# Optimization experiments

Measured on AMD Instinct MI355X. Metric: run time of the kernel, lower is better.

Reference implementation:

```python
import jax, jax.numpy as jnp
import numpy as np
import math

H = 128
NUM_RBF = 32
CUTOFF_UPPER = 4.5
CUTOFF_LOWER = 0.0
N_NODES = 16384
N_EDGES = 65536
EPS = 1e-5


def _layernorm(x, gamma, beta):
    m = x.mean(-1, keepdims=True)
    v = ((x - m) ** 2).mean(-1, keepdims=True)
    return (x - m) / jnp.sqrt(v + EPS) * gamma + beta


def _cosine_cutoff(d):
    # cutoff_lower == 0 branch of CosineCutoff
    return 0.5 * (jnp.cos(d * (math.pi / CUTOFF_UPPER)) + 1.0) * (d < CUTOFF_UPPER).astype(d.dtype)


def _expnorm_rbf(d):
    alpha = 5.0 / (CUTOFF_UPPER - CUTOFF_LOWER)
    start = math.exp(-CUTOFF_UPPER + CUTOFF_LOWER)
    means = jnp.linspace(start, 1.0, NUM_RBF, dtype=d.dtype)
    betas = jnp.full((NUM_RBF,), (2.0 / NUM_RBF * (1.0 - start)) ** -2, dtype=d.dtype)
    de = d[:, None]
    return _cosine_cutoff(de) * jnp.exp(-betas * (jnp.exp(alpha * (-de + CUTOFF_LOWER)) - means) ** 2)


def _skew(v):  # [E,3] -> [E,3,3]
    z = jnp.zeros(v.shape[0], v.dtype)
    return jnp.stack([z, -v[:, 2], v[:, 1], v[:, 2], z, -v[:, 0], -v[:, 1], v[:, 0], z], axis=1).reshape(-1, 3, 3)


def _sym(v):  # traceless symmetric part of outer product, [E,3] -> [E,3,3]
    M = v[:, :, None] * v[:, None, :]
    tr3 = (v * v).sum(-1)[:, None, None] / 3.0
    return M - tr3 * jnp.eye(3, dtype=v.dtype)


def _tensor_norm(T):  # [...,3,3] -> [...]
    return (T ** 2).sum((-2, -1))


def setup_inputs() -> dict:
    key = jax.random.key(0)
    ks = jax.random.split(key, 32)
    s = 0.05
    inp = {
        'z': jax.random.randint(ks[0], (N_NODES,), 0, 128, dtype=jnp.int32),
        'pos': jax.random.normal(ks[1], (N_NODES, 3), jnp.float32) * 3.0,
        'batch': jnp.zeros((N_NODES,), jnp.int32),
        'edge_index': jax.random.randint(ks[2], (2, N_EDGES), 0, N_NODES, dtype=jnp.int64),
        'emb_w': jax.random.normal(ks[3], (128, H), jnp.float32) * s,
        'emb2_w': jax.random.normal(ks[4], (H, 2 * H), jnp.float32) * s,
        'emb2_b': jnp.zeros((H,), jnp.float32),
        'dp1_w': jax.random.normal(ks[5], (H, NUM_RBF), jnp.float32) * s,
        'dp1_b': jnp.zeros((H,), jnp.float32),
        'dp2_w': jax.random.normal(ks[6], (H, NUM_RBF), jnp.float32) * s,
        'dp2_b': jnp.zeros((H,), jnp.float32),
        'dp3_w': jax.random.normal(ks[7], (H, NUM_RBF), jnp.float32) * s,
        'dp3_b': jnp.zeros((H,), jnp.float32),
        'lt0_w': jax.random.normal(ks[8], (H, H), jnp.float32) * s,
        'lt1_w': jax.random.normal(ks[9], (H, H), jnp.float32) * s,
        'lt2_w': jax.random.normal(ks[10], (H, H), jnp.float32) * s,
        'ls0_w': jax.random.normal(ks[11], (2 * H, H), jnp.float32) * s,
        'ls0_b': jnp.zeros((2 * H,), jnp.float32),
        'ls1_w': jax.random.normal(ks[12], (3 * H, 2 * H), jnp.float32) * s,
        'ls1_b': jnp.zeros((3 * H,), jnp.float32),
        'in_gamma': jnp.ones((H,), jnp.float32),
        'in_beta': jnp.zeros((H,), jnp.float32),
        'lin_w': jax.random.normal(ks[13], (H, 3 * H), jnp.float32) * s,
        'lin_b': jnp.zeros((H,), jnp.float32),
        'on_gamma': jnp.ones((3 * H,), jnp.float32),
        'on_beta': jnp.zeros((3 * H,), jnp.float32),
        'ol1_w': jax.random.normal(ks[14], (H // 2, H), jnp.float32) * s,
        'ol1_b': jnp.zeros((H // 2,), jnp.float32),
        'ol2_w': jax.random.normal(ks[15], (1, H // 2), jnp.float32) * s,
        'ol2_b': jnp.zeros((1,), jnp.float32),
    }
    return inp


def reference(z, pos, batch, edge_index, emb_w, emb2_w, emb2_b, dp1_w, dp1_b, dp2_w, dp2_b,
              dp3_w, dp3_b, lt0_w, lt1_w, lt2_w, ls0_w, ls0_b, ls1_w, ls1_b,
              in_gamma, in_beta, lin_w, lin_b, on_gamma, on_beta, ol1_w, ol1_b, ol2_w, ol2_b):
    src, dst = edge_index[0], edge_index[1]
    edge_vec = pos[src] - pos[dst]                            # [E,3]
    edge_weight = jnp.sqrt((edge_vec ** 2).sum(-1))           # [E]
    edge_attr = _expnorm_rbf(edge_weight)                     # [E,R]
    self_mask = src == dst
    edge_vec_norm = edge_vec / jnp.where(self_mask, 1.0, edge_weight)[:, None]

    # atomic-number message: Zij = emb2(concat(emb[z_src], emb[z_dst]))
    Zemb = emb_w[z]                                           # [N,H]
    Zcat = jnp.concatenate([Zemb[src], Zemb[dst]], axis=-1)   # [E,2H]
    Zij = Zcat @ emb2_w.T + emb2_b                            # [E,H]

    C = (_cosine_cutoff(edge_weight)[:, None] * Zij)[:, :, None, None]  # [E,H,1,1]
    eye = jnp.eye(3, dtype=pos.dtype)[None, None]
    d1 = (edge_attr @ dp1_w.T + dp1_b)[:, :, None, None]      # [E,H,1,1]
    d2 = (edge_attr @ dp2_w.T + dp2_b)[:, :, None, None]
    d3 = (edge_attr @ dp3_w.T + dp3_b)[:, :, None, None]
    Iij = d1 * C * eye                                        # [E,H,3,3]
    Aij = d2 * C * _skew(edge_vec_norm)[:, None, :, :]
    Sij = d3 * C * _sym(edge_vec_norm)[:, None, :, :]

    N = pos.shape[0]
    I0 = jax.ops.segment_sum(Iij, src, num_segments=N)        # [N,H,3,3]
    A0 = jax.ops.segment_sum(Aij, src, num_segments=N)
    S0 = jax.ops.segment_sum(Sij, src, num_segments=N)

    tnorm = _layernorm(_tensor_norm(I0 + A0 + S0), in_gamma, in_beta)  # [N,H]
    nrm = jax.nn.silu(tnorm @ ls0_w.T + ls0_b)
    nrm = jax.nn.silu(nrm @ ls1_w.T + ls1_b).reshape(-1, H, 3)          # [N,H,3]

    I = jnp.einsum('nhij,kh->nkij', I0, lt0_w) * nrm[:, :, 0, None, None]
    A = jnp.einsum('nhij,kh->nkij', A0, lt1_w) * nrm[:, :, 1, None, None]
    S = jnp.einsum('nhij,kh->nkij', S0, lt2_w) * nrm[:, :, 2, None, None]

    x = jnp.concatenate([_tensor_norm(I), _tensor_norm(A), _tensor_norm(S)], axis=-1)  # [N,3H]
    x = _layernorm(x, on_gamma, on_beta)
    x = jax.nn.silu(x @ lin_w.T + lin_b)                       # [N,H]
    x = jax.nn.silu(x @ ol1_w.T + ol1_b)                       # [N,H//2]
    y = x @ ol2_w.T + ol2_b                                    # [N,1] per-atom scalar
    return y
```

## Files before the change

### kernel.cpp

```cpp
#include <hip/hip_runtime.h>
#include <math.h>

#define NN 16384
#define NE 65536
#define HH 128

constexpr double D_START = 0.011108996538242306;
constexpr double D_STEP  = (1.0 - D_START) / 31.0;
constexpr float  F_ALPHA = (float)(5.0/4.5);
constexpr double D_BB    = (2.0/32.0)*(1.0 - D_START);
constexpr float  F_BETA  = (float)(1.0/(D_BB*D_BB));
constexpr float  F_PIC   = (float)(M_PI/4.5);

#define POOL_BYTES (16u*1024u*1024u)
__device__ __align__(256) static char g_pool[POOL_BYTES];

typedef __attribute__((ext_vector_type(8))) short bf16x8;
typedef __attribute__((ext_vector_type(4))) float f32x4;

__device__ __forceinline__ float siluf(float x){
  return x * (1.0f/(1.0f + expf(-x)));
}
__device__ __forceinline__ short f2bf(float x){
  unsigned u = __float_as_uint(x);
  unsigned r = (u + 0x7fffu + ((u>>16)&1u)) >> 16;
  return (short)r;
}
__device__ __forceinline__ float bf2f(short h){
  return __uint_as_float(((unsigned)(unsigned short)h)<<16);
}
__device__ __forceinline__ void split_bf(float x, short& h, short& l){
  h = f2bf(x);
  l = f2bf(x - bf2f(h));
}

__global__ __launch_bounds__(256) void k_prep(
    const int* __restrict__ ei, const float* __restrict__ pos,
    const int* __restrict__ z,
    const float* __restrict__ emb_w, const float* __restrict__ emb2_w,
    const float* __restrict__ emb2_b,
    const float* __restrict__ ls0, const float* __restrict__ ls1,
    const float* __restrict__ lin, const float* __restrict__ lt0,
    const float* __restrict__ lt1, const float* __restrict__ lt2,
    const float* __restrict__ dp1, const float* __restrict__ dp2,
    const float* __restrict__ dp3, const float* __restrict__ ol1,
    float* __restrict__ PZ, float* __restrict__ QZ,
    int* __restrict__ bcnt, int* __restrict__ bucket,
    int* __restrict__ ezs, int* __restrict__ ezd, float* __restrict__ ev,
    short* __restrict__ atth, short* __restrict__ attl,
    short* __restrict__ ls0h, short* __restrict__ ls0l,
    short* __restrict__ ls1h, short* __restrict__ ls1l,
    short* __restrict__ linh, short* __restrict__ linl,
    short* __restrict__ lt0h, short* __restrict__ lt0l,
    short* __restrict__ lt1h, short* __restrict__ lt1l,
    short* __restrict__ lt2h, short* __restrict__ lt2l,
    short* __restrict__ dwh, short* __restrict__ dwl,
    short* __restrict__ ol1h, short* __restrict__ ol1l){
  int b = blockIdx.x;
  if (b < 64){
    __shared__ float erow[2][128];
    int sub = threadIdx.x >> 7, h = threadIdx.x & 127;
    int a = b*2 + sub;
    erow[sub][h] = emb_w[a*128 + h];
    __syncthreads();
    float p = 0.f, q = 0.f;
    #pragma unroll 8
    for (int k=0;k<128;++k){
      float e = erow[sub][k];
      p += e * emb2_w[h*256 + k];
      q += e * emb2_w[h*256 + 128 + k];
    }
    PZ[a*128 + h] = p + emb2_b[h];
    QZ[a*128 + h] = q;
    return;
  }
  if (b < 1040){
    int tid = (b-64)*256 + threadIdx.x;
    const float* s; short *dh, *dl; int i;
    if      (tid < 32768)  { s=ls0; dh=ls0h; dl=ls0l; i=tid; }
    else if (tid < 131072) { s=ls1; dh=ls1h; dl=ls1l; i=tid-32768; }
    else if (tid < 180224) { s=lin; dh=linh; dl=linl; i=tid-131072; }
    else if (tid < 196608) { s=lt0; dh=lt0h; dl=lt0l; i=tid-180224; }
    else if (tid < 212992) { s=lt1; dh=lt1h; dl=lt1l; i=tid-196608; }
    else if (tid < 229376) { s=lt2; dh=lt2h; dl=lt2l; i=tid-212992; }
    else if (tid < 241664) {
      int j = tid - 229376;
      int g = j >> 12, idx = j & 4095;
      s = (g==0)?dp1:((g==1)?dp2:dp3);
      short h,l; split_bf(s[idx], h, l);
      dwh[j] = h; dwl[j] = l;
      return;
    }
    else { s=ol1; dh=ol1h; dl=ol1l; i=tid-241664; }
    short h,l; split_bf(s[i], h, l);
    dh[i] = h; dl[i] = l;
    return;
  }
  {
    int e = (b-1040)*256 + threadIdx.x;
    int s = ei[e];
    int t = ei[NE + e];
    float dx = pos[3*s+0] - pos[3*t+0];
    float dy = pos[3*s+1] - pos[3*t+1];
    float dz = pos[3*s+2] - pos[3*t+2];
    float d = sqrtf(dx*dx + dy*dy + dz*dz);
    if (d < 4.5f){
      int g16 = s >> 4;
      int p = atomicAdd(&bcnt[g16], 1);
      if (p < 512) bucket[g16*512 + p] = (e<<4) | (s & 15);
      ezs[e] = z[s];
      ezd[e] = z[t];
      float denom = (s==t) ? 1.0f : d;
      ev[4*e+0] = dx/denom;
      ev[4*e+1] = dy/denom;
      ev[4*e+2] = dz/denom;
      float cut = 0.5f*(cosf(d*F_PIC) + 1.0f);
      ev[4*e+3] = cut;
      float q = expf(-F_ALPHA*d);
      #pragma unroll
      for (int r=0;r<32;++r){
        float m = (float)(D_START + r*D_STEP);
        float u = q - m;
        float a = cut * expf(-F_BETA*u*u);
        short hh, ll; split_bf(a, hh, ll);
        atth[32*e + r] = hh;
        attl[32*e + r] = ll;
      }
    }
  }
}

__global__ __launch_bounds__(256, 2) void k_mega(
    const int* __restrict__ bcnt, const int* __restrict__ bucket,
    const int* __restrict__ ezs, const int* __restrict__ ezd,
    const float* __restrict__ ev,
    const short* __restrict__ atth, const short* __restrict__ attl,
    const short* __restrict__ dwh, const short* __restrict__ dwl,
    const float* __restrict__ db1, const float* __restrict__ db2,
    const float* __restrict__ db3,
    const float* __restrict__ PZ, const float* __restrict__ QZ,
    const float* __restrict__ in_g, const float* __restrict__ in_b,
    const short* __restrict__ w0h, const short* __restrict__ w0l,
    const short* __restrict__ w1h, const short* __restrict__ w1l,
    const short* __restrict__ w2h, const short* __restrict__ w2l,
    const short* __restrict__ ls0h, const short* __restrict__ ls0l,
    const float* __restrict__ ls0b,
    const short* __restrict__ ls1h, const short* __restrict__ ls1l,
    const float* __restrict__ ls1b,
    const short* __restrict__ linh, const short* __restrict__ linl,
    const float* __restrict__ linb,
    const short* __restrict__ ol1h, const short* __restrict__ ol1l,
    const float* __restrict__ ol1b,
    const float* __restrict__ ol2w, const float* __restrict__ ol2b,
    const float* __restrict__ on_g, const float* __restrict__ on_b,
    float* __restrict__ y){
  __shared__ __align__(16) char sm[76288];
  float* Dt    = (float*)sm;
  int*   elocal= (int*)(sm + 24832);
  int*   tmpb  = (int*)(sm + 26880);
  int*   lcnt  = (int*)(sm + 28928);
  int*   loff  = lcnt + 16;
  int*   lcur  = loff + 17;
  short* PlnL  = (short*)sm;
  short* T1h   = (short*)sm;
  short* T1l   = (short*)(sm + 9216);
  float* xls   = (float*)sm;
  short* X3h   = (short*)sm;
  short* X3l   = (short*)(sm + 5120);
  float* partL = (float*)(sm + 10240);
  short* tnhL  = (short*)(sm + 51200);
  short* tnlL  = (short*)(sm + 51200 + 5120);
  float* NRMt  = (float*)(sm + 51200);
  short* xhL   = (short*)(sm + 51200);
  short* xlL   = (short*)(sm + 51200 + 12544);

  int t = threadIdx.x;
  int b = blockIdx.x;
  int w = t >> 6, lane = t & 63;
  int col16 = lane & 15, quad = lane >> 4;
  int bn = b*16;
  int node = t >> 4, q = t & 15;

  int ecnt = bcnt[b]; if (ecnt > 512) ecnt = 512;
  if (t < 16){ lcnt[t] = 0; lcur[t] = 0; }
  __syncthreads();
  for (int j = t; j < ecnt; j += 256){
    int val = bucket[b*512 + j];
    tmpb[j] = val;
    atomicAdd(&lcnt[val & 15], 1);
  }
  __syncthreads();
  if (t == 0){
    int a = 0;
    #pragma unroll
    for (int i=0;i<16;++i){ loff[i] = a; a += lcnt[i]; }
    loff[16] = a;
  }
  __syncthreads();
  for (int j = t; j < ecnt; j += 256){
    int val = tmpb[j];
    int nd = val & 15;
    int p = loff[nd] + atomicAdd(&lcur[nd], 1);
    elocal[p] = val >> 4;
  }
  __syncthreads();
  int etot = loff[16];
  int e0n = loff[node], e1n = loff[node+1];

  float pv[10][8];
  #pragma unroll
  for (int p=0;p<10;++p)
    #pragma unroll
    for (int i=0;i<8;++i) pv[p][i]=0.f;

  const float* dbp[3] = {db1, db2, db3};
  for (int c0 = 0; c0 < etot; c0 += 16){
    int jA = c0 + col16; if (jA >= etot) jA = etot - 1;
    int eA = elocal[jA];
    bf16x8 ah = *(const bf16x8*)(atth + (size_t)eA*32 + quad*8);
    bf16x8 al = *(const bf16x8*)(attl + (size_t)eA*32 + quad*8);
    f32x4 dacc[6];
    #pragma unroll
    for (int nt=0;nt<6;++nt) dacc[nt] = (f32x4){0.f,0.f,0.f,0.f};
    #pragma unroll
    for (int nt=0;nt<6;++nt){
      int col = w*96 + nt*16 + col16;
      int g = col >> 7, cg = col & 127;
      bf16x8 wh = *(const bf16x8*)(dwh + g*4096 + cg*32 + quad*8);
      bf16x8 wl = *(const bf16x8*)(dwl + g*4096 + cg*32 + quad*8);
      dacc[nt] = __builtin_amdgcn_mfma_f32_16x16x32_bf16(ah, wh, dacc[nt], 0,0,0);
      dacc[nt] = __builtin_amdgcn_mfma_f32_16x16x32_bf16(ah, wl, dacc[nt], 0,0,0);
      dacc[nt] = __builtin_amdgcn_mfma_f32_16x16x32_bf16(al, wh, dacc[nt], 0,0,0);
    }
    #pragma unroll
    for (int nt=0;nt<6;++nt){
      int col = w*96 + nt*16 + col16;
      int g = col >> 7;
      float bb = dbp[g][col & 127];
      #pragma unroll
      for (int r=0;r<4;++r)
        Dt[(quad*4+r)*388 + col] = dacc[nt][r] + bb;
    }
    __syncthreads();
    int jlo = e0n > c0 ? e0n : c0;
    int jhi0 = c0 + 16; if (jhi0 > etot) jhi0 = etot;
    int jhi = e1n < jhi0 ? e1n : jhi0;
    for (int j = jlo; j < jhi; ++j){
      int le = j - c0;
      int e = elocal[j];
      float4 evv = *(const float4*)(ev + 4*e);
      int zs = ezs[e], zd = ezd[e];
      const float* pz = PZ + zs*128 + q*8;
      const float* qz = QZ + zd*128 + q*8;
      const float* dr = Dt + le*388 + q*8;
      float vx = evv.x, vy = evv.y, vz = evv.z, cut = evv.w;
      float t3v = (vx*vx + vy*vy + vz*vz)*(1.0f/3.0f);
      #pragma unroll
      for (int i=0;i<8;++i){
        float C = cut * (pz[i] + qz[i]);
        float d1 = dr[i], d2 = dr[128+i], d3 = dr[256+i];
        pv[0][i] += d1*C;
        float wa = d2*C;
        pv[1][i] += wa*vx; pv[2][i] += wa*vy; pv[3][i] += wa*vz;
        float ws = d3*C;
        pv[4][i] += ws*(vx*vx - t3v);
        pv[5][i] += ws*(vy*vy - t3v);
        pv[6][i] += ws*(vz*vz - t3v);
        pv[7][i] += ws*(vx*vy);
        pv[8][i] += ws*(vx*vz);
        pv[9][i] += ws*(vy*vz);
      }
    }
    __syncthreads();
  }

  {
    float tnv[8];
    float s8 = 0.f;
    #pragma unroll
    for (int i=0;i<8;++i){
      float x = 3.f*pv[0][i]*pv[0][i]
              + 2.f*(pv[1][i]*pv[1][i]+pv[2][i]*pv[2][i]+pv[3][i]*pv[3][i])
              + (pv[4][i]*pv[4][i]+pv[5][i]*pv[5][i]+pv[6][i]*pv[6][i])
              + 2.f*(pv[7][i]*pv[7][i]+pv[8][i]*pv[8][i]+pv[9][i]*pv[9][i]);
      tnv[i] = x; s8 += x;
    }
    #pragma unroll
    for (int o=8;o;o>>=1) s8 += __shfl_xor(s8, o, 64);
    float mean = s8*(1.0f/128.0f);
    float vq = 0.f;
    #pragma unroll
    for (int i=0;i<8;++i){ float d = tnv[i]-mean; vq += d*d; }
    #pragma unroll
    for (int o=8;o;o>>=1) vq += __shfl_xor(vq, o, 64);
    float rstd = 1.0f/sqrtf(vq*(1.0f/128.0f) + 1e-5f);
    #pragma unroll
    for (int i=0;i<8;++i){
      int h = q*8 + i;
      float val = (tnv[i]-mean)*rstd*in_g[h] + in_b[h];
      short hh, ll; split_bf(val, hh, ll);
      tnhL[node*160 + h] = hh;
      tnlL[node*160 + h] = ll;
    }
  }

  const short* wgh[3] = {w0h, w1h, w2h};
  const short* wgl[3] = {w0l, w1l, w2l};
  constexpr int gmap[10] = {0,1,1,1,2,2,2,2,2,2};
  f32x4 acc[10][2];
  #pragma unroll
  for (int pass=0; pass<2; ++pass){
    int pbase = pass*5;
    __syncthreads();
    #pragma unroll
    for (int pl=0; pl<5; ++pl){
      short* dst = PlnL + (pl*4 + (q>>2))*1280 + node*80 + (q&3)*16;
      #pragma unroll
      for (int i=0;i<8;++i){
        short hh, ll; split_bf(pv[pbase+pl][i], hh, ll);
        dst[i] = hh; dst[8+i] = ll;
      }
    }
    __syncthreads();
    #pragma unroll
    for (int pl=0; pl<5; ++pl)
      #pragma unroll
      for (int tt=0; tt<2; ++tt) acc[pbase+pl][tt] = (f32x4){0.f,0.f,0.f,0.f};
    #pragma unroll
    for (int hc4=0; hc4<4; ++hc4){
      bf16x8 bh[2], bl[2];
      int curg = -1;
      #pragma unroll
      for (int pl=0; pl<5; ++pl){
        int p = pbase + pl;
        const int g = gmap[p];
        if (g != curg){
          #pragma unroll
          for (int tt=0; tt<2; ++tt){
            int row = w*32 + tt*16 + col16;
            bh[tt] = *(const bf16x8*)(wgh[g] + row*128 + hc4*32 + quad*8);
            bl[tt] = *(const bf16x8*)(wgl[g] + row*128 + hc4*32 + quad*8);
          }
          curg = g;
        }
        const short* ab = PlnL + (pl*4 + hc4)*1280 + col16*80 + quad*16;
        bf16x8 ah = *(const bf16x8*)(ab);
        bf16x8 al = *(const bf16x8*)(ab + 8);
        #pragma unroll
        for (int tt=0; tt<2; ++tt){
          acc[p][tt] = __builtin_amdgcn_mfma_f32_16x16x32_bf16(ah, bh[tt], acc[p][tt], 0,0,0);
          acc[p][tt] = __builtin_amdgcn_mfma_f32_16x16x32_bf16(ah, bl[tt], acc[p][tt], 0,0,0);
          acc[p][tt] = __builtin_amdgcn_mfma_f32_16x16x32_bf16(al, bh[tt], acc[p][tt], 0,0,0);
        }
      }
    }
  }
  __syncthreads();

  {
    f32x4 macc[4];
    #pragma unroll
    for (int nt=0;nt<4;++nt) macc[nt] = (f32x4){0.f,0.f,0.f,0.f};
    #pragma unroll
    for (int kc=0; kc<4; ++kc){
      bf16x8 tah = *(const bf16x8*)(tnhL + col16*160 + kc*32 + quad*8);
      bf16x8 tal = *(const bf16x8*)(tnlL + col16*160 + kc*32 + quad*8);
      #pragma unroll
      for (int nt=0;nt<4;++nt){
        int n = w*64 + nt*16 + col16;
        bf16x8 wh = *(const bf16x8*)(ls0h + n*128 + kc*32 + quad*8);
        bf16x8 wl = *(const bf16x8*)(ls0l + n*128 + kc*32 + quad*8);
        macc[nt] = __builtin_amdgcn_mfma_f32_16x16x32_bf16(tah, wh, macc[nt], 0,0,0);
        macc[nt] = __builtin_amdgcn_mfma_f32_16x16x32_bf16(tah, wl, macc[nt], 0,0,0);
        macc[nt] = __builtin_amdgcn_mfma_f32_16x16x32_bf16(tal, wh, macc[nt], 0,0,0);
      }
    }
    __syncthreads();
    #pragma unroll
    for (int nt=0;nt<4;++nt){
      int n = w*64 + nt*16 + col16;
      float bb = ls0b[n];
      #pragma unroll
      for (int r=0;r<4;++r){
        float v = siluf(macc[nt][r] + bb);
        short hh, ll; split_bf(v, hh, ll);
        T1h[(quad*4+r)*288 + n] = hh;
        T1l[(quad*4+r)*288 + n] = ll;
      }
    }
    __syncthreads();
    f32x4 nacc[6];
    #pragma unroll
    for (int nt=0;nt<6;++nt) nacc[nt] = (f32x4){0.f,0.f,0.f,0.f};
    #pragma unroll
    for (int kc=0; kc<8; ++kc){
      bf16x8 tah = *(const bf16x8*)(T1h + col16*288 + kc*32 + quad*8);
      bf16x8 tal = *(const bf16x8*)(T1l + col16*288 + kc*32 + quad*8);
      #pragma unroll
      for (int nt=0;nt<6;++nt){
        int n = w*96 + nt*16 + col16;
        bf16x8 wh = *(const bf16x8*)(ls1h + n*256 + kc*32 + quad*8);
        bf16x8 wl = *(const bf16x8*)(ls1l + n*256 + kc*32 + quad*8);
        nacc[nt] = __builtin_amdgcn_mfma_f32_16x16x32_bf16(tah, wh, nacc[nt], 0,0,0);
        nacc[nt] = __builtin_amdgcn_mfma_f32_16x16x32_bf16(tah, wl, nacc[nt], 0,0,0);
        nacc[nt] = __builtin_amdgcn_mfma_f32_16x16x32_bf16(tal, wh, nacc[nt], 0,0,0);
      }
    }
    __syncthreads();
    #pragma unroll
    for (int nt=0;nt<6;++nt){
      int n = w*96 + nt*16 + col16;
      float bb = ls1b[n];
      #pragma unroll
      for (int r=0;r<4;++r)
        NRMt[(quad*4+r)*388 + n] = siluf(nacc[nt][r] + bb);
    }
    __syncthreads();
  }

  #pragma unroll
  for (int tt=0; tt<2; ++tt){
    int k = w*32 + tt*16 + col16;
    #pragma unroll
    for (int r=0; r<4; ++r){
      int nloc = quad*4 + r;
      const float* nr = NRMt + nloc*388 + 3*k;
      float n0 = nr[0], n1 = nr[1], n2 = nr[2];
      float tI = acc[0][tt][r]*n0;
      float xI = 3.f*tI*tI;
      float a0 = acc[1][tt][r]*n1, a1 = acc[2][tt][r]*n1, a2 = acc[3][tt][r]*n1;
      float xA = 2.f*(a0*a0 + a1*a1 + a2*a2);
      float d0 = acc[4][tt][r]*n2, d1 = acc[5][tt][r]*n2, d2 = acc[6][tt][r]*n2;
      float o0 = acc[7][tt][r]*n2, o1 = acc[8][tt][r]*n2, o2 = acc[9][tt][r]*n2;
      float xS = d0*d0 + d1*d1 + d2*d2 + 2.f*(o0*o0 + o1*o1 + o2*o2);
      xls[nloc*388 + k]       = xI;
      xls[nloc*388 + 128 + k] = xA;
      xls[nloc*388 + 256 + k] = xS;
    }
  }
  __syncthreads();

  {
    float vv[24];
    float s = 0.f;
    #pragma unroll
    for (int i=0;i<24;++i){ vv[i] = xls[node*388 + q*24 + i]; s += vv[i]; }
    #pragma unroll
    for (int o=8;o;o>>=1) s += __shfl_xor(s, o, 64);
    float mean = s*(1.0f/384.0f);
    float qsum = 0.f;
    #pragma unroll
    for (int i=0;i<24;++i){ float d = vv[i]-mean; qsum += d*d; }
    #pragma unroll
    for (int o=8;o;o>>=1) qsum += __shfl_xor(qsum, o, 64);
    float rstd = 1.0f/sqrtf(qsum*(1.0f/384.0f) + 1e-5f);
    #pragma unroll
    for (int i=0;i<24;++i){
      int c = q*24 + i;
      float val = (vv[i]-mean)*rstd*on_g[c] + on_b[c];
      short hh, ll; split_bf(val, hh, ll);
      xhL[node*392 + c] = hh;
      xlL[node*392 + c] = ll;
    }
  }
  __syncthreads();

  {
    f32x4 lacc[2];
    #pragma unroll
    for (int nt=0;nt<2;++nt) lacc[nt] = (f32x4){0.f,0.f,0.f,0.f};
    #pragma unroll
    for (int kc=0; kc<12; ++kc){
      bf16x8 xah = *(const bf16x8*)(xhL + col16*392 + kc*32 + quad*8);
      bf16x8 xal = *(const bf16x8*)(xlL + col16*392 + kc*32 + quad*8);
      #pragma unroll
      for (int nt=0;nt<2;++nt){
        int n = w*32 + nt*16 + col16;
        bf16x8 wh = *(const bf16x8*)(linh + n*384 + kc*32 + quad*8);
        bf16x8 wl = *(const bf16x8*)(linl + n*384 + kc*32 + quad*8);
        lacc[nt] = __builtin_amdgcn_mfma_f32_16x16x32_bf16(xah, wh, lacc[nt], 0,0,0);
        lacc[nt] = __builtin_amdgcn_mfma_f32_16x16x32_bf16(xah, wl, lacc[nt], 0,0,0);
        lacc[nt] = __builtin_amdgcn_mfma_f32_16x16x32_bf16(xal, wh, lacc[nt], 0,0,0);
      }
    }
    __syncthreads();
    #pragma unroll
    for (int nt=0;nt<2;++nt){
      int n = w*32 + nt*16 + col16;
      float bb = linb[n];
      #pragma unroll
      for (int r=0;r<4;++r){
        float v = siluf(lacc[nt][r] + bb);
        short hh, ll; split_bf(v, hh, ll);
        X3h[(quad*4+r)*160 + n] = hh;
        X3l[(quad*4+r)*160 + n] = ll;
      }
    }
    __syncthreads();
  }

  {
    f32x4 hacc = (f32x4){0.f,0.f,0.f,0.f};
    int n = w*16 + col16;
    #pragma unroll
    for (int kc=0; kc<4; ++kc){
      bf16x8 xah = *(const bf16x8*)(X3h + col16*160 + kc*32 + quad*8);
      bf16x8 xal = *(const bf16x8*)(X3l + col16*160 + kc*32 + quad*8);
      bf16x8 wh = *(const bf16x8*)(ol1h + n*128 + kc*32 + quad*8);
      bf16x8 wl = *(const bf16x8*)(ol1l + n*128 + kc*32 + quad*8);
      hacc = __builtin_amdgcn_mfma_f32_16x16x32_bf16(xah, wh, hacc, 0,0,0);
      hacc = __builtin_amdgcn_mfma_f32_16x16x32_bf16(xah, wl, hacc, 0,0,0);
      hacc = __builtin_amdgcn_mfma_f32_16x16x32_bf16(xal, wh, hacc, 0,0,0);
    }
    float b1 = ol1b[n], w2 = ol2w[n];
    #pragma unroll
    for (int r=0;r<4;++r){
      float v = siluf(hacc[r] + b1) * w2;
      #pragma unroll
      for (int o=8;o;o>>=1) v += __shfl_xor(v, o, 64);
      if (col16 == 0) partL[w*16 + quad*4 + r] = v;
    }
    __syncthreads();
    if (t < 16)
      y[bn + t] = partL[t] + partL[16+t] + partL[32+t] + partL[48+t] + ol2b[0];
  }
}

extern "C" void kernel_launch(void* const* d_in, const int* in_sizes, int n_in,
                              void* d_out, int out_size, void* d_ws, size_t ws_size,
                              hipStream_t stream) {
  const int*   z      = (const int*)d_in[0];
  const float* pos    = (const float*)d_in[1];
  const int*   ei     = (const int*)d_in[3];
  const float* emb_w  = (const float*)d_in[4];
  const float* emb2_w = (const float*)d_in[5];
  const float* emb2_b = (const float*)d_in[6];
  const float* dp1_w  = (const float*)d_in[7];
  const float* dp1_b  = (const float*)d_in[8];
  const float* dp2_w  = (const float*)d_in[9];
  const float* dp2_b  = (const float*)d_in[10];
  const float* dp3_w  = (const float*)d_in[11];
  const float* dp3_b  = (const float*)d_in[12];
  const float* lt0_w  = (const float*)d_in[13];
  const float* lt1_w  = (const float*)d_in[14];
  const float* lt2_w  = (const float*)d_in[15];
  const float* ls0_w  = (const float*)d_in[16];
  const float* ls0_b  = (const float*)d_in[17];
  const float* ls1_w  = (const float*)d_in[18];
  const float* ls1_b  = (const float*)d_in[19];
  const float* in_g   = (const float*)d_in[20];
  const float* in_b   = (const float*)d_in[21];
  const float* lin_w  = (const float*)d_in[22];
  const float* lin_b  = (const float*)d_in[23];
  const float* on_g   = (const float*)d_in[24];
  const float* on_b   = (const float*)d_in[25];
  const float* ol1_w  = (const float*)d_in[26];
  const float* ol1_b  = (const float*)d_in[27];
  const float* ol2_w  = (const float*)d_in[28];
  const float* ol2_b  = (const float*)d_in[29];
  float* out = (float*)d_out;

  const size_t NEED = 14u*1024u*1024u;
  char* wsb = (char*)d_ws;
  if (ws_size < NEED){
    void* p = nullptr;
    hipGetSymbolAddress(&p, HIP_SYMBOL(g_pool));
    wsb = (char*)p;
  }
  size_t off = 0;
  auto alloc = [&](size_t bytes)->void*{
    void* p = wsb + off;
    off = (off + bytes + 255) & ~(size_t)255;
    return p;
  };
  float* PZ      = (float*)alloc(128*128*4);
  float* QZ      = (float*)alloc(128*128*4);
  int*   bcnt    = (int*)  alloc(1024*4);
  int*   bucket  = (int*)  alloc((size_t)1024*512*4);
  int*   ezs     = (int*)  alloc(NE*4);
  int*   ezd     = (int*)  alloc(NE*4);
  float* ev      = (float*)alloc((size_t)NE*4*4);
  short* atth    = (short*)alloc((size_t)NE*32*2);
  short* attl    = (short*)alloc((size_t)NE*32*2);
  short* dwh     = (short*)alloc(3*128*32*2);
  short* dwl     = (short*)alloc(3*128*32*2);
  short* ls0h    = (short*)alloc(256*128*2);
  short* ls0l    = (short*)alloc(256*128*2);
  short* ls1h    = (short*)alloc(384*256*2);
  short* ls1l    = (short*)alloc(384*256*2);
  short* linh    = (short*)alloc(128*384*2);
  short* linl    = (short*)alloc(128*384*2);
  short* lt0h    = (short*)alloc(128*128*2);
  short* lt0l    = (short*)alloc(128*128*2);
  short* lt1h    = (short*)alloc(128*128*2);
  short* lt1l    = (short*)alloc(128*128*2);
  short* lt2h    = (short*)alloc(128*128*2);
  short* lt2l    = (short*)alloc(128*128*2);
  short* ol1h    = (short*)alloc(64*128*2);
  short* ol1l    = (short*)alloc(64*128*2);

  hipMemsetAsync(bcnt, 0, 1024*4, stream);

  k_prep<<<1296, 256, 0, stream>>>(ei, pos, z, emb_w, emb2_w, emb2_b,
                                   ls0_w, ls1_w, lin_w, lt0_w, lt1_w, lt2_w,
                                   dp1_w, dp2_w, dp3_w, ol1_w,
                                   PZ, QZ, bcnt, bucket, ezs, ezd, ev, atth, attl,
                                   ls0h, ls0l, ls1h, ls1l, linh, linl,
                                   lt0h, lt0l, lt1h, lt1l, lt2h, lt2l,
                                   dwh, dwl, ol1h, ol1l);
  k_mega<<<NN/16, 256, 0, stream>>>(bcnt, bucket, ezs, ezd, ev, atth, attl,
                                    dwh, dwl, dp1_b, dp2_b, dp3_b,
                                    PZ, QZ, in_g, in_b,
                                    lt0h, lt0l, lt1h, lt1l, lt2h, lt2l,
                                    ls0h, ls0l, ls0_b, ls1h, ls1l, ls1_b,
                                    linh, linl, lin_b, ol1h, ol1l, ol1_b,
                                    ol2_w, ol2_b, on_g, on_b, out);
}
```

Baseline: 266.9 us.

## Reorder norm MLP before tensor GEMMs to shrink LDS and registers

Moves the ls0/ls1 MLP that produces the norm factors ahead of the per-component tensor linear GEMMs. Each GEMM pass's accumulators can then be reduced immediately into running xI/xA/xS sums instead of keeping all 10 accumulator planes live. Shared memory drops from about 76KB to 53KB by overlapping buffers, and launch bounds go from 2 to 3 blocks per CU to raise occupancy. The cost is five plane-staging passes instead of two, so more barriers, and register pressure may force spills.

```diff
diff --git a/kernel.cpp b/kernel.cpp
--- a/kernel.cpp
+++ b/kernel.cpp
@@ -130,7 +130,7 @@
   }
 }
 
-__global__ __launch_bounds__(256, 2) void k_mega(
+__global__ __launch_bounds__(256, 3) void k_mega(
     const int* __restrict__ bcnt, const int* __restrict__ bucket,
     const int* __restrict__ ezs, const int* __restrict__ ezd,
     const float* __restrict__ ev,
@@ -154,25 +154,25 @@
     const float* __restrict__ ol2w, const float* __restrict__ ol2b,
     const float* __restrict__ on_g, const float* __restrict__ on_b,
     float* __restrict__ y){
-  __shared__ __align__(16) char sm[76288];
+  __shared__ __align__(16) char sm[53248];
   float* Dt    = (float*)sm;
   int*   elocal= (int*)(sm + 24832);
-  int*   tmpb  = (int*)(sm + 26880);
-  int*   lcnt  = (int*)(sm + 28928);
+  int*   lcnt  = (int*)(sm + 26880);
   int*   loff  = lcnt + 16;
   int*   lcur  = loff + 17;
-  short* PlnL  = (short*)sm;
   short* T1h   = (short*)sm;
   short* T1l   = (short*)(sm + 9216);
+  short* PlnL  = (short*)sm;
   float* xls   = (float*)sm;
   short* X3h   = (short*)sm;
   short* X3l   = (short*)(sm + 5120);
   float* partL = (float*)(sm + 10240);
-  short* tnhL  = (short*)(sm + 51200);
-  short* tnlL  = (short*)(sm + 51200 + 5120);
-  float* NRMt  = (float*)(sm + 51200);
-  short* xhL   = (short*)(sm + 51200);
-  short* xlL   = (short*)(sm + 51200 + 12544);
+  int*   tmpb  = (int*)(sm + 28160);
+  short* tnhL  = (short*)(sm + 28160);
+  short* tnlL  = (short*)(sm + 28160 + 5120);
+  float* NRMt  = (float*)(sm + 28160);
+  short* xhL   = (short*)(sm + 28160);
+  short* xlL   = (short*)(sm + 28160 + 12544);
 
   int t = threadIdx.x;
   int b = blockIdx.x;
@@ -303,17 +303,80 @@
       tnlL[node*160 + h] = ll;
     }
   }
+  __syncthreads();
+
+  {
+    f32x4 macc[4];
+    #pragma unroll
+    for (int nt=0;nt<4;++nt) macc[nt] = (f32x4){0.f,0.f,0.f,0.f};
+    #pragma unroll
+    for (int kc=0; kc<4; ++kc){
+      bf16x8 tah = *(const bf16x8*)(tnhL + col16*160 + kc*32 + quad*8);
+      bf16x8 tal = *(const bf16x8*)(tnlL + col16*160 + kc*32 + quad*8);
+      #pragma unroll
+      for (int nt=0;nt<4;++nt){
+        int n = w*64 + nt*16 + col16;
+        bf16x8 wh = *(const bf16x8*)(ls0h + n*128 + kc*32 + quad*8);
+        bf16x8 wl = *(const bf16x8*)(ls0l + n*128 + kc*32 + quad*8);
+        macc[nt] = __builtin_amdgcn_mfma_f32_16x16x32_bf16(tah, wh, macc[nt], 0,0,0);
+        macc[nt] = __builtin_amdgcn_mfma_f32_16x16x32_bf16(tah, wl, macc[nt], 0,0,0);
+        macc[nt] = __builtin_amdgcn_mfma_f32_16x16x32_bf16(tal, wh, macc[nt], 0,0,0);
+      }
+    }
+    #pragma unroll
+    for (int nt=0;nt<4;++nt){
+      int n = w*64 + nt*16 + col16;
+      float bb = ls0b[n];
+      #pragma unroll
+      for (int r=0;r<4;++r){
+        float v = siluf(macc[nt][r] + bb);
+        short hh, ll; split_bf(v, hh, ll);
+        T1h[(quad*4+r)*288 + n] = hh;
+        T1l[(quad*4+r)*288 + n] = ll;
+      }
+    }
+    __syncthreads();
+    f32x4 nacc[6];
+    #pragma unroll
+    for (int nt=0;nt<6;++nt) nacc[nt] = (f32x4){0.f,0.f,0.f,0.f};
+    #pragma unroll
+    for (int kc=0; kc<8; ++kc){
+      bf16x8 tah = *(const bf16x8*)(T1h + col16*288 + kc*32 + quad*8);
+      bf16x8 tal = *(const bf16x8*)(T1l + col16*288 + kc*32 + quad*8);
+      #pragma unroll
+      for (int nt=0;nt<6;++nt){
+        int n = w*96 + nt*16 + col16;
+        bf16x8 wh = *(const bf16x8*)(ls1h + n*256 + kc*32 + quad*8);
+        bf16x8 wl = *(const bf16x8*)(ls1l + n*256 + kc*32 + quad*8);
+        nacc[nt] = __builtin_amdgcn_mfma_f32_16x16x32_bf16(tah, wh, nacc[nt], 0,0,0);
+        nacc[nt] = __builtin_amdgcn_mfma_f32_16x16x32_bf16(tah, wl, nacc[nt], 0,0,0);
+        nacc[nt] = __builtin_amdgcn_mfma_f32_16x16x32_bf16(tal, wh, nacc[nt], 0,0,0);
+      }
+    }
+    __syncthreads();
+    #pragma unroll
+    for (int nt=0;nt<6;++nt){
+      int n = w*96 + nt*16 + col16;
+      float bb = ls1b[n];
+      #pragma unroll
+      for (int r=0;r<4;++r)
+        NRMt[(quad*4+r)*388 + n] = siluf(nacc[nt][r] + bb);
+    }
+  }
 
   const short* wgh[3] = {w0h, w1h, w2h};
   const short* wgl[3] = {w0l, w1l, w2l};
-  constexpr int gmap[10] = {0,1,1,1,2,2,2,2,2,2};
-  f32x4 acc[10][2];
+  float xI[2][4], xA[2][4], xS[2][4];
   #pragma unroll
-  for (int pass=0; pass<2; ++pass){
-    int pbase = pass*5;
-    __syncthreads();
-    #pragma unroll
-    for (int pl=0; pl<5; ++pl){
+  for (int tt=0;tt<2;++tt)
+    #pragma unroll
+    for (int r=0;r<4;++r){ xI[tt][r]=0.f; xA[tt][r]=0.f; xS[tt][r]=0.f; }
+  #pragma unroll
+  for (int pass=0; pass<5; ++pass){
+    const int pbase = pass*2;
+    __syncthreads();
+    #pragma unroll
+    for (int pl=0; pl<2; ++pl){
       short* dst = PlnL + (pl*4 + (q>>2))*1280 + node*80 + (q&3)*16;
       #pragma unroll
       for (int i=0;i<8;++i){
@@ -322,18 +385,19 @@
       }
     }
     __syncthreads();
-    #pragma unroll
-    for (int pl=0; pl<5; ++pl)
-      #pragma unroll
-      for (int tt=0; tt<2; ++tt) acc[pbase+pl][tt] = (f32x4){0.f,0.f,0.f,0.f};
+    f32x4 acc[2][2];
+    #pragma unroll
+    for (int pl=0;pl<2;++pl)
+      #pragma unroll
+      for (int tt=0;tt<2;++tt) acc[pl][tt] = (f32x4){0.f,0.f,0.f,0.f};
     #pragma unroll
     for (int hc4=0; hc4<4; ++hc4){
       bf16x8 bh[2], bl[2];
       int curg = -1;
       #pragma unroll
-      for (int pl=0; pl<5; ++pl){
-        int p = pbase + pl;
-        const int g = gmap[p];
+      for (int pl=0; pl<2; ++pl){
+        const int p = pbase + pl;
+        const int g = (p==0)?0:((p<4)?1:2);
         if (g != curg){
           #pragma unroll
           for (int tt=0; tt<2; ++tt){
@@ -348,75 +412,33 @@
         bf16x8 al = *(const bf16x8*)(ab + 8);
         #pragma unroll
         for (int tt=0; tt<2; ++tt){
-          acc[p][tt] = __builtin_amdgcn_mfma_f32_16x16x32_bf16(ah, bh[tt], acc[p][tt], 0,0,0);
-          acc[p][tt] = __builtin_amdgcn_mfma_f32_16x16x32_bf16(ah, bl[tt], acc[p][tt], 0,0,0);
-          acc[p][tt] = __builtin_amdgcn_mfma_f32_16x16x32_bf16(al, bh[tt], acc[p][tt], 0,0,0);
+          acc[pl][tt] = __builtin_amdgcn_mfma_f32_16x16x32_bf16(ah, bh[tt], acc[pl][tt], 0,0,0);
+          acc[pl][tt] = __builtin_amdgcn_mfma_f32_16x16x32_bf16(ah, bl[tt], acc[pl][tt], 0,0,0);
+          acc[pl][tt] = __builtin_amdgcn_mfma_f32_16x16x32_bf16(al, bh[tt], acc[pl][tt], 0,0,0);
         }
       }
     }
-  }
-  __syncthreads();
-
-  {
-    f32x4 macc[4];
-    #pragma unroll
-    for (int nt=0;nt<4;++nt) macc[nt] = (f32x4){0.f,0.f,0.f,0.f};
-    #pragma unroll
-    for (int kc=0; kc<4; ++kc){
-      bf16x8 tah = *(const bf16x8*)(tnhL + col16*160 + kc*32 + quad*8);
-      bf16x8 tal = *(const bf16x8*)(tnlL + col16*160 + kc*32 + quad*8);
-      #pragma unroll
-      for (int nt=0;nt<4;++nt){
-        int n = w*64 + nt*16 + col16;
-        bf16x8 wh = *(const bf16x8*)(ls0h + n*128 + kc*32 + quad*8);
-        bf16x8 wl = *(const bf16x8*)(ls0l + n*128 + kc*32 + quad*8);
-        macc[nt] = __builtin_amdgcn_mfma_f32_16x16x32_bf16(tah, wh, macc[nt], 0,0,0);
-        macc[nt] = __builtin_amdgcn_mfma_f32_16x16x32_bf16(tah, wl, macc[nt], 0,0,0);
-        macc[nt] = __builtin_amdgcn_mfma_f32_16x16x32_bf16(tal, wh, macc[nt], 0,0,0);
-      }
-    }
-    __syncthreads();
-    #pragma unroll
-    for (int nt=0;nt<4;++nt){
-      int n = w*64 + nt*16 + col16;
-      float bb = ls0b[n];
-      #pragma unroll
-      for (int r=0;r<4;++r){
-        float v = siluf(macc[nt][r] + bb);
-        short hh, ll; split_bf(v, hh, ll);
-        T1h[(quad*4+r)*288 + n] = hh;
-        T1l[(quad*4+r)*288 + n] = ll;
-      }
-    }
-    __syncthreads();
-    f32x4 nacc[6];
-    #pragma unroll
-    for (int nt=0;nt<6;++nt) nacc[nt] = (f32x4){0.f,0.f,0.f,0.f};
-    #pragma unroll
-    for (int kc=0; kc<8; ++kc){
-      bf16x8 tah = *(const bf16x8*)(T1h + col16*288 + kc*32 + quad*8);
-      bf16x8 tal = *(const bf16x8*)(T1l + col16*288 + kc*32 + quad*8);
-      #pragma unroll
-      for (int nt=0;nt<6;++nt){
-        int n = w*96 + nt*16 + col16;
-        bf16x8 wh = *(const bf16x8*)(ls1h + n*256 + kc*32 + quad*8);
-        bf16x8 wl = *(const bf16x8*)(ls1l + n*256 + kc*32 + quad*8);
-        nacc[nt] = __builtin_amdgcn_mfma_f32_16x16x32_bf16(tah, wh, nacc[nt], 0,0,0);
-        nacc[nt] = __builtin_amdgcn_mfma_f32_16x16x32_bf16(tah, wl, nacc[nt], 0,0,0);
-        nacc[nt] = __builtin_amdgcn_mfma_f32_16x16x32_bf16(tal, wh, nacc[nt], 0,0,0);
-      }
-    }
-    __syncthreads();
-    #pragma unroll
-    for (int nt=0;nt<6;++nt){
-      int n = w*96 + nt*16 + col16;
-      float bb = ls1b[n];
-      #pragma unroll
-      for (int r=0;r<4;++r)
-        NRMt[(quad*4+r)*388 + n] = siluf(nacc[nt][r] + bb);
-    }
-    __syncthreads();
-  }
+    #pragma unroll
+    for (int pl=0; pl<2; ++pl){
+      const int p = pbase + pl;
+      const int sel = (p==0)?0:((p<4)?1:2);
+      #pragma unroll
+      for (int tt=0; tt<2; ++tt){
+        int k = w*32 + tt*16 + col16;
+        #pragma unroll
+        for (int r=0; r<4; ++r){
+          int nloc = quad*4 + r;
+          float n = NRMt[nloc*388 + 3*k + sel];
+          float v = acc[pl][tt][r]*n;
+          if (p==0)      xI[tt][r]  = 3.f*v*v;
+          else if (p<4)  xA[tt][r] += 2.f*v*v;
+          else if (p<7)  xS[tt][r] += v*v;
+          else           xS[tt][r] += 2.f*v*v;
+        }
+      }
+    }
+  }
+  __syncthreads();
 
   #pragma unroll
   for (int tt=0; tt<2; ++tt){
@@ -424,22 +446,12 @@
     #pragma unroll
     for (int r=0; r<4; ++r){
       int nloc = quad*4 + r;
-      const float* nr = NRMt + nloc*388 + 3*k;
-      float n0 = nr[0], n1 = nr[1], n2 = nr[2];
-      float tI = acc[0][tt][r]*n0;
-      float xI = 3.f*tI*tI;
-      float a0 = acc[1][tt][r]*n1, a1 = acc[2][tt][r]*n1, a2 = acc[3][tt][r]*n1;
-      float xA = 2.f*(a0*a0 + a1*a1 + a2*a2);
-      float d0 = acc[4][tt][r]*n2, d1 = acc[5][tt][r]*n2, d2 = acc[6][tt][r]*n2;
-      float o0 = acc[7][tt][r]*n2, o1 = acc[8][tt][r]*n2, o2 = acc[9][tt][r]*n2;
-      float xS = d0*d0 + d1*d1 + d2*d2 + 2.f*(o0*o0 + o1*o1 + o2*o2);
-      xls[nloc*388 + k]       = xI;
-      xls[nloc*388 + 128 + k] = xA;
-      xls[nloc*388 + 256 + k] = xS;
-    }
-  }
-  __syncthreads();
-
+      xls[nloc*388 + k]       = xI[tt][r];
+      xls[nloc*388 + 128 + k] = xA[tt][r];
+      xls[nloc*388 + 256 + k] = xS[tt][r];
+    }
+  }
+  __syncthreads();
   {
     float vv[24];
     float s = 0.f;
```

New measurement: 327.7 us. 22.8% more time.
